# Performance work log

Measured on AMD Instinct MI355X. Metric: run time of the kernel, lower is better.

Reference implementation:

```python
import jax, jax.numpy as jnp
import numpy as np
from jax import lax

B, W, K = 64, 128, 64      # batch, window_size, n_features
KS = 7                      # conv kernel size
EF = W                      # feature-attn embed dim (defaults to window_size, GATv1)
ET = 2 * K                  # temporal-attn embed dim (n_features doubled by GATv2)
H = 256                     # GRU hidden
FH = 256                    # forecast MLP hidden
ALPHA = 0.2                 # leaky relu slope


def _leaky(v):
    return jnp.where(v >= 0, v, ALPHA * v)


def setup_inputs() -> dict:
    key = jax.random.key(0)
    ks = jax.random.split(key, 20)
    s = 0.05
    inp = {
        "x": jax.random.normal(ks[0], (B, W, K), jnp.float32),
        # ConvLayer
        "conv_w": jax.random.normal(ks[1], (K, K, KS), jnp.float32) * s,
        "conv_b": jnp.zeros((K,), jnp.float32),
        # FeatureAttentionLayer (GATv1): lin W->EF, a:[2EF,1], bias [K,K]
        "feat_lin_w": jax.random.normal(ks[2], (EF, W), jnp.float32) * s,
        "feat_lin_b": jnp.zeros((EF,), jnp.float32),
        "feat_a": jax.random.normal(ks[3], (2 * EF, 1), jnp.float32) * s,
        "feat_bias": jnp.zeros((K, K), jnp.float32),
        # TemporalAttentionLayer (GATv2): lin 2K->ET, a:[ET,1], bias [W,W]
        "temp_lin_w": jax.random.normal(ks[4], (ET, 2 * K), jnp.float32) * s,
        "temp_lin_b": jnp.zeros((ET,), jnp.float32),
        "temp_a": jax.random.normal(ks[5], (ET, 1), jnp.float32) * s,
        "temp_bias": jnp.zeros((W, W), jnp.float32),
        # GRU (1 layer), input dim 3K
        "gru_wih": jax.random.normal(ks[6], (3 * H, 3 * K), jnp.float32) * s,
        "gru_whh": jax.random.normal(ks[7], (3 * H, H), jnp.float32) * s,
        "gru_bih": jnp.zeros((3 * H,), jnp.float32),
        "gru_bhh": jnp.zeros((3 * H,), jnp.float32),
        "fc0_w": jax.random.normal(ks[8], (FH, H), jnp.float32) * s,
        "fc0_b": jnp.zeros((FH,), jnp.float32),
        "fc1_w": jax.random.normal(ks[9], (FH, FH), jnp.float32) * s,
        "fc1_b": jnp.zeros((FH,), jnp.float32),
        "fc2_w": jax.random.normal(ks[10], (FH, FH), jnp.float32) * s,
        "fc2_b": jnp.zeros((FH,), jnp.float32),
        "fc3_w": jax.random.normal(ks[11], (K, FH), jnp.float32) * s,
        "fc3_b": jnp.zeros((K,), jnp.float32),
    }
    return inp


def _forward(x, conv_w, conv_b, feat_lin_w, feat_lin_b, feat_a, feat_bias,
             temp_lin_w, temp_lin_b, temp_a, temp_bias,
             gru_wih, gru_whh, gru_bih, gru_bhh,
             fc0_w, fc0_b, fc1_w, fc1_b, fc2_w, fc2_b, fc3_w, fc3_b):
    # --- ConvLayer: pad (k-1)//2 both sides, Conv1d K->K, ReLU ---
    pad = (KS - 1) // 2
    xc = x.transpose(0, 2, 1)                                   # [B,K,W]
    xc = jnp.pad(xc, ((0, 0), (0, 0), (pad, pad)))
    y = lax.conv_general_dilated(xc, conv_w, (1,), 'VALID',
                                 dimension_numbers=('NCH', 'OIH', 'NCH'))
    y = jax.nn.relu(y + conv_b[None, :, None]).transpose(0, 2, 1)  # [B,W,K]

    # --- FeatureAttentionLayer (GATv1): e_ij = leaky((Wx_i||Wx_j)·a) ---
    xf = y.transpose(0, 2, 1)                                   # [B,K,W]
    Wx = xf @ feat_lin_w.T + feat_lin_b                         # [B,K,EF]
    s1 = Wx @ feat_a[:EF, 0]                                    # [B,K]
    s2 = Wx @ feat_a[EF:, 0]                                    # [B,K]
    e_f = _leaky(s1[:, :, None] + s2[:, None, :]) + feat_bias   # [B,K,K]
    att_f = jax.nn.softmax(e_f, axis=2)
    h_feat = jax.nn.sigmoid(att_f @ xf).transpose(0, 2, 1)      # [B,W,K]

    # --- TemporalAttentionLayer (GATv2): g = leaky(lin(x_i||x_j)); e = g·a ---
    W1, W2 = temp_lin_w[:, :K], temp_lin_w[:, K:]               # split lin over concat halves
    p = y @ W1.T                                                # [B,W,ET]
    q = y @ W2.T                                                # [B,W,ET]
    g = _leaky(p[:, :, None, :] + q[:, None, :, :] + temp_lin_b)  # [B,W,W,ET]
    e_t = (g @ temp_a)[..., 0] + temp_bias                      # [B,W,W]
    att_t = jax.nn.softmax(e_t, axis=2)
    h_temp = jax.nn.sigmoid(att_t @ y)                          # [B,W,K]

    # --- concat + GRU over time ---
    z = jnp.concatenate([y, h_feat, h_temp], axis=2)            # [B,W,3K]

    def gru_step(h, xt):
        gi = xt @ gru_wih.T + gru_bih                           # [B,3H]
        gh = h @ gru_whh.T + gru_bhh
        ir, iz, inn = jnp.split(gi, 3, axis=1)
        hr, hz, hn = jnp.split(gh, 3, axis=1)
        r = jax.nn.sigmoid(ir + hr)
        zg = jax.nn.sigmoid(iz + hz)
        n = jnp.tanh(inn + r * hn)
        return (1.0 - zg) * n + zg * h, None

    h0 = jnp.zeros((z.shape[0], H), z.dtype)
    h_end, _ = lax.scan(gru_step, h0, z.transpose(1, 0, 2))     # [B,H]

    # --- Forecasting MLP (eval mode: dropout is identity) ---
    v = jax.nn.relu(h_end @ fc0_w.T + fc0_b)
    v = jax.nn.relu(v @ fc1_w.T + fc1_b)
    v = jax.nn.relu(v @ fc2_w.T + fc2_b)
    return v @ fc3_w.T + fc3_b                                  # [B,K]


def reference(x, conv_w, conv_b, feat_lin_w, feat_lin_b, feat_a, feat_bias,
              temp_lin_w, temp_lin_b, temp_a, temp_bias,
              gru_wih, gru_whh, gru_bih, gru_bhh,
              fc0_w, fc0_b, fc1_w, fc1_b, fc2_w, fc2_b, fc3_w, fc3_b):
    return _forward(x, conv_w, conv_b, feat_lin_w, feat_lin_b, feat_a, feat_bias,
                    temp_lin_w, temp_lin_b, temp_a, temp_bias,
                    gru_wih, gru_whh, gru_bih, gru_bhh,
                    fc0_w, fc0_b, fc1_w, fc1_b, fc2_w, fc2_b, fc3_w, fc3_b)
```

## Files before the change

### kernel.cpp

```cpp
#include <hip/hip_runtime.h>
#include <hip/hip_bf16.h>

typedef unsigned int uint;
typedef _Float16 half2_t __attribute__((ext_vector_type(2)));
typedef _Float16 half8 __attribute__((ext_vector_type(8)));
typedef float f32x4 __attribute__((ext_vector_type(4)));

union H2U { uint u; half2_t h; };
union U4H8 { uint4 u; half8 h; };

#define OFF_Y    0u
#define OFF_Z    524288u
#define OFF_GI   2097152u
#define OFF_WHH  8388608u
#define OFF_C12  8486912u
#define OFF_DD   8487168u
#define OFF_HEND 8487424u

__global__ __launch_bounds__(256) void k_pack_prep(const float* __restrict__ whh, uint* __restrict__ w16,
                                                   const float* __restrict__ flw, const float* __restrict__ flb,
                                                   const float* __restrict__ fa, float* __restrict__ c12,
                                                   float* __restrict__ dd) {
    __shared__ float red[256];
    int bx = blockIdx.x, tid = threadIdx.x;
    if (bx < 384) {
        int idx = bx * 256 + tid;
        int tidq = idx / 384;
        int rem = idx - tidq * 384;
        int u = rem >> 5;
        int q = (rem >> 2) & 7;
        int p = rem & 3;
        int w = tidq >> 6, l = tidq & 63;
        int row = w * 192 + u * 16 + (l & 15);
        int colb = q * 32 + (l >> 4) * 8 + 2 * p;
        float a = whh[(size_t)row * 256 + colb];
        float b = whh[(size_t)row * 256 + colb + 1];
        H2U uu; uu.h.x = (_Float16)a; uu.h.y = (_Float16)b;
        w16[idx] = uu.u;
    } else {
        if (tid < 128) {
            float a = 0.f, b = 0.f;
            for (int e = 0; e < 128; ++e) {
                float w = flw[e * 128 + tid];
                a = fmaf(w, fa[e], a);
                b = fmaf(w, fa[128 + e], b);
            }
            c12[tid] = a;
            c12[128 + tid] = b;
        }
        int e = tid & 127;
        red[tid] = (tid < 128) ? flb[e] * fa[e] : flb[e] * fa[128 + e];
        __syncthreads();
        if (tid < 2) {
            float s = 0.f;
            for (int q = 0; q < 128; ++q) s += red[tid * 128 + q];
            dd[tid] = s;
        }
    }
}

__global__ __launch_bounds__(256) void k_conv(const float* __restrict__ x, const float* __restrict__ cw,
                                              const float* __restrict__ cb, float* __restrict__ y,
                                              float* __restrict__ z) {
    __shared__ float xT[64][41];
    __shared__ float cwL[64 * 64 * 7];
    int b = blockIdx.y, w0 = blockIdx.x * 32, tid = threadIdx.x;
    for (int idx = tid; idx < 38 * 64; idx += 256) {
        int wl = idx / 64, k = idx % 64;
        int wg = w0 - 3 + wl;
        xT[k][wl] = (wg >= 0 && wg < 128) ? x[((size_t)b * 128 + wg) * 64 + k] : 0.f;
    }
    for (int idx = tid; idx < 64 * 64 * 7; idx += 256) cwL[idx] = cw[idx];
    __syncthreads();
    int w_l = tid % 32, kog = tid / 32;
    float acc[8];
#pragma unroll
    for (int i = 0; i < 8; ++i) acc[i] = 0.f;
    for (int ki = 0; ki < 64; ++ki) {
        float x7[7];
#pragma unroll
        for (int u = 0; u < 7; ++u) x7[u] = xT[ki][w_l + u];
#pragma unroll
        for (int koi = 0; koi < 8; ++koi) {
            const float* wp = &cwL[((kog * 8 + koi) * 64 + ki) * 7];
#pragma unroll
            for (int u = 0; u < 7; ++u) acc[koi] = fmaf(x7[u], wp[u], acc[koi]);
        }
    }
    int w = w0 + w_l;
#pragma unroll
    for (int koi = 0; koi < 8; ++koi) {
        int ko = kog * 8 + koi;
        float v = acc[koi] + cb[ko];
        v = v > 0.f ? v : 0.f;
        y[((size_t)b * 128 + w) * 64 + ko] = v;
        z[((size_t)b * 128 + w) * 192 + ko] = v;
    }
}

__global__ __launch_bounds__(256) void k_feat(const float* __restrict__ y, const float* __restrict__ c12,
                                              const float* __restrict__ dd, const float* __restrict__ fb,
                                              float* __restrict__ z) {
    int b = blockIdx.y, w0 = blockIdx.x * 32, tid = threadIdx.x;
    __shared__ float s1L[64], s2L[64];
    __shared__ float attL[64][65];
    __shared__ float yL[32][64];
    __shared__ float cL[256];
    cL[tid] = c12[tid];
    for (int idx = tid; idx < 32 * 64; idx += 256) {
        int wl = idx / 64, j = idx % 64;
        yL[wl][j] = y[((size_t)b * 128 + w0 + wl) * 64 + j];
    }
    __syncthreads();
    if (tid < 128) {
        int k = tid % 64;
        const float* c = (tid < 64) ? cL : cL + 128;
        float acc = 0.f;
        for (int w = 0; w < 128; ++w) acc = fmaf(y[((size_t)b * 128 + w) * 64 + k], c[w], acc);
        if (tid < 64) s1L[k] = acc + dd[0]; else s2L[k] = acc + dd[1];
    }
    __syncthreads();
    if (tid < 64) {
        int k = tid;
        float s1 = s1L[k];
        float m = -1e30f;
        for (int j = 0; j < 64; ++j) {
            float v = s1 + s2L[j];
            float l = fmaxf(v, 0.2f * v);
            float e = l + fb[k * 64 + j];
            attL[k][j] = e;
            m = fmaxf(m, e);
        }
        float s = 0.f;
        for (int j = 0; j < 64; ++j) { float e = __expf(attL[k][j] - m); attL[k][j] = e; s += e; }
        float inv = 1.f / s;
        for (int j = 0; j < 64; ++j) attL[k][j] *= inv;
    }
    __syncthreads();
    int k_l = tid % 64, wg = tid / 64;
    for (int wi = 0; wi < 8; ++wi) {
        int wl = wg * 8 + wi;
        float acc = 0.f;
#pragma unroll 16
        for (int j = 0; j < 64; ++j) acc = fmaf(attL[k_l][j], yL[wl][j], acc);
        float hv = 1.f / (1.f + __expf(-acc));
        z[((size_t)b * 128 + w0 + wl) * 192 + 64 + k_l] = hv;
    }
}

__global__ __launch_bounds__(512) void k_temp(const float* __restrict__ y, const float* __restrict__ tlw,
                                              const float* __restrict__ tlb, const float* __restrict__ ta,
                                              const float* __restrict__ tbias, float* __restrict__ z) {
    int b = blockIdx.y, i0 = blockIdx.x * 32, tid = threadIdx.x;
    __shared__ __align__(16) float yT[64][132];
    __shared__ __align__(16) float qL[128][128];
    __shared__ __align__(16) float pL[32][128];
    __shared__ __align__(16) float etL[32][128];
    __shared__ __align__(16) float taL[128];
    __shared__ float mred[32][8], sred[32][8];
    __shared__ float mrow[32], invL[32];
    if (tid < 128) taL[tid] = ta[tid];
    for (int idx = tid; idx < 8192; idx += 512) {
        int j = idx >> 6, k = idx & 63;
        yT[k][j] = y[((size_t)b * 128 + j) * 64 + k];
    }
    __syncthreads();
    {
        int c = tid & 127, ih = tid >> 7;
        float w1r[64];
        const float4* w1p = (const float4*)(tlw + c * 128);
#pragma unroll
        for (int q4 = 0; q4 < 16; ++q4) {
            float4 v = w1p[q4];
            w1r[4 * q4] = v.x; w1r[4 * q4 + 1] = v.y; w1r[4 * q4 + 2] = v.z; w1r[4 * q4 + 3] = v.w;
        }
        float base = tlb[c];
#pragma unroll
        for (int ilb = 0; ilb < 2; ++ilb) {
            int j0 = i0 + ih * 8 + ilb * 4;
            float4 acc = {base, base, base, base};
            for (int k = 0; k < 64; ++k) {
                float4 yv = *((const float4*)&yT[k][j0]);
                float w = w1r[k];
                acc.x = fmaf(yv.x, w, acc.x); acc.y = fmaf(yv.y, w, acc.y);
                acc.z = fmaf(yv.z, w, acc.z); acc.w = fmaf(yv.w, w, acc.w);
            }
            int il = ih * 8 + ilb * 4;
            pL[il][c] = acc.x; pL[il + 1][c] = acc.y; pL[il + 2][c] = acc.z; pL[il + 3][c] = acc.w;
        }
    }
    {
        int j = tid & 127, ch = tid >> 7;
        float yreg[64];
#pragma unroll
        for (int k = 0; k < 64; ++k) yreg[k] = yT[k][j];
        for (int cc = 0; cc < 32; ++cc) {
            int c = __builtin_amdgcn_readfirstlane(ch * 32 + cc);
            const float* w2 = tlw + c * 128 + 64;
            float acc = 0.f;
#pragma unroll
            for (int k = 0; k < 64; ++k) acc = fmaf(yreg[k], w2[k], acc);
            qL[c][j] = acc;
        }
    }
    __syncthreads();
    {
        int jg = tid & 31, ih = tid >> 5;
        int j0 = jg * 4;
        int il0 = ih * 2;
        float4 acc0 = *((const float4*)(tbias + (size_t)(i0 + il0) * 128 + j0));
        float4 acc1 = *((const float4*)(tbias + (size_t)(i0 + il0 + 1) * 128 + j0));
        for (int c0 = 0; c0 < 128; c0 += 4) {
            float4 ta4 = *((const float4*)&taL[c0]);
            float4 p0 = *((const float4*)&pL[il0][c0]);
            float4 p1 = *((const float4*)&pL[il0 + 1][c0]);
            float4 q0 = *((const float4*)&qL[c0 + 0][j0]);
            float4 q1 = *((const float4*)&qL[c0 + 1][j0]);
            float4 q2 = *((const float4*)&qL[c0 + 2][j0]);
            float4 q3 = *((const float4*)&qL[c0 + 3][j0]);
#define ETSTEP(qv, tac, pa, pb) { \
            float u; \
            u = (pa) + qv.x; acc0.x = fmaf(fmaxf(u, 0.2f * u), (tac), acc0.x); \
            u = (pa) + qv.y; acc0.y = fmaf(fmaxf(u, 0.2f * u), (tac), acc0.y); \
            u = (pa) + qv.z; acc0.z = fmaf(fmaxf(u, 0.2f * u), (tac), acc0.z); \
            u = (pa) + qv.w; acc0.w = fmaf(fmaxf(u, 0.2f * u), (tac), acc0.w); \
            u = (pb) + qv.x; acc1.x = fmaf(fmaxf(u, 0.2f * u), (tac), acc1.x); \
            u = (pb) + qv.y; acc1.y = fmaf(fmaxf(u, 0.2f * u), (tac), acc1.y); \
            u = (pb) + qv.z; acc1.z = fmaf(fmaxf(u, 0.2f * u), (tac), acc1.z); \
            u = (pb) + qv.w; acc1.w = fmaf(fmaxf(u, 0.2f * u), (tac), acc1.w); }
            ETSTEP(q0, ta4.x, p0.x, p1.x)
            ETSTEP(q1, ta4.y, p0.y, p1.y)
            ETSTEP(q2, ta4.z, p0.z, p1.z)
            ETSTEP(q3, ta4.w, p0.w, p1.w)
#undef ETSTEP
        }
        *((float4*)&etL[il0][j0]) = acc0;
        *((float4*)&etL[il0 + 1][j0]) = acc1;
    }
    __syncthreads();
    if (tid < 256) {
        int il = tid >> 3, seg = tid & 7;
        const float4* ep = (const float4*)&etL[il][seg * 16];
        float m = -1e30f;
#pragma unroll
        for (int q = 0; q < 4; ++q) {
            float4 e = ep[q];
            m = fmaxf(m, fmaxf(fmaxf(e.x, e.y), fmaxf(e.z, e.w)));
        }
        mred[il][seg] = m;
    }
    __syncthreads();
    if (tid < 32) {
        float m = mred[tid][0];
#pragma unroll
        for (int s = 1; s < 8; ++s) m = fmaxf(m, mred[tid][s]);
        mrow[tid] = m;
    }
    __syncthreads();
    if (tid < 256) {
        int il = tid >> 3, seg = tid & 7;
        float m = mrow[il];
        float4* ep = (float4*)&etL[il][seg * 16];
        float s = 0.f;
#pragma unroll
        for (int q = 0; q < 4; ++q) {
            float4 e = ep[q];
            e.x = __expf(e.x - m); e.y = __expf(e.y - m);
            e.z = __expf(e.z - m); e.w = __expf(e.w - m);
            s += (e.x + e.y) + (e.z + e.w);
            ep[q] = e;
        }
        sred[il][seg] = s;
    }
    __syncthreads();
    if (tid < 32) {
        float s = 0.f;
#pragma unroll
        for (int q = 0; q < 8; ++q) s += sred[tid][q];
        invL[tid] = 1.f / s;
    }
    __syncthreads();
    {
        int k = tid & 63, ig = tid >> 6;
        float acc[4] = {0.f, 0.f, 0.f, 0.f};
        const float* yb = y + (size_t)b * 128 * 64 + k;
        for (int j0 = 0; j0 < 128; j0 += 4) {
            float yv[4];
#pragma unroll
            for (int jj = 0; jj < 4; ++jj) yv[jj] = yb[(size_t)(j0 + jj) * 64];
#pragma unroll
            for (int ii = 0; ii < 4; ++ii) {
                int il = ig * 4 + ii;
                float4 ev = *((const float4*)&etL[il][j0]);
                acc[ii] = fmaf(ev.x, yv[0], acc[ii]);
                acc[ii] = fmaf(ev.y, yv[1], acc[ii]);
                acc[ii] = fmaf(ev.z, yv[2], acc[ii]);
                acc[ii] = fmaf(ev.w, yv[3], acc[ii]);
            }
        }
#pragma unroll
        for (int ii = 0; ii < 4; ++ii) {
            int il = ig * 4 + ii;
            float hv = 1.f / (1.f + __expf(-acc[ii] * invL[il]));
            z[((size_t)b * 128 + i0 + il) * 192 + 128 + k] = hv;
        }
    }
}

__global__ __launch_bounds__(256) void k_gi(const float* __restrict__ z, const float* __restrict__ wih,
                                            const float* __restrict__ bih, float* __restrict__ gi) {
    int o0 = blockIdx.x * 128;
    int bt0 = blockIdx.y * 64;
    int tid = threadIdx.x;
    __shared__ __align__(16) float zL[64][68];
    __shared__ float wL[128][65];
    int ol = tid & 31;
    int r8 = (tid >> 5) * 8;
    float acc[8][4];
#pragma unroll
    for (int rr = 0; rr < 8; ++rr)
#pragma unroll
        for (int oo = 0; oo < 4; ++oo) acc[rr][oo] = 0.f;
    for (int mc = 0; mc < 3; ++mc) {
        int m0 = mc * 64;
        __syncthreads();
        {
            int mq = (tid & 15) * 4;
            int r = tid >> 4;
#pragma unroll
            for (int it = 0; it < 4; ++it, r += 16) {
                float4 v = *((const float4*)&z[(size_t)(bt0 + r) * 192 + m0 + mq]);
                *((float4*)&zL[r][mq]) = v;
            }
            int o = tid >> 4;
#pragma unroll
            for (int it = 0; it < 8; ++it, o += 16) {
                float4 v = *((const float4*)&wih[(size_t)(o0 + o) * 192 + m0 + mq]);
                wL[o][mq] = v.x; wL[o][mq + 1] = v.y; wL[o][mq + 2] = v.z; wL[o][mq + 3] = v.w;
            }
        }
        __syncthreads();
        for (int mb = 0; mb < 64; mb += 4) {
            float4 zv[8];
#pragma unroll
            for (int rr = 0; rr < 8; ++rr) zv[rr] = *((const float4*)&zL[r8 + rr][mb]);
#pragma unroll
            for (int mi = 0; mi < 4; ++mi) {
                float wv[4];
#pragma unroll
                for (int oo = 0; oo < 4; ++oo) wv[oo] = wL[ol + 32 * oo][mb + mi];
#pragma unroll
                for (int rr = 0; rr < 8; ++rr) {
                    float zc = (mi == 0) ? zv[rr].x : (mi == 1) ? zv[rr].y : (mi == 2) ? zv[rr].z : zv[rr].w;
#pragma unroll
                    for (int oo = 0; oo < 4; ++oo) acc[rr][oo] = fmaf(zc, wv[oo], acc[rr][oo]);
                }
            }
        }
    }
    float bo[4];
#pragma unroll
    for (int oo = 0; oo < 4; ++oo) bo[oo] = bih[o0 + ol + 32 * oo];
#pragma unroll
    for (int rr = 0; rr < 8; ++rr)
#pragma unroll
        for (int oo = 0; oo < 4; ++oo)
            gi[(size_t)(bt0 + r8 + rr) * 768 + o0 + ol + 32 * oo] = acc[rr][oo] + bo[oo];
}

__global__ __launch_bounds__(256)
__attribute__((amdgpu_waves_per_eu(1, 1)))
void k_gru(const float* __restrict__ gi,
           const uint* __restrict__ w16,
           const float* __restrict__ bhh,
           float* __restrict__ hend) {
    int b = blockIdx.x, tid = threadIdx.x;
    int w = tid >> 6, l = tid & 63;
    int quad = l >> 4;
    __shared__ __align__(16) _Float16 hp16[256];
    __shared__ float sH[768];
    half8 bfr[96];
    {
        const uint4* wp4 = (const uint4*)(w16 + (size_t)tid * 384);
#pragma unroll
        for (int i = 0; i < 96; ++i) { U4H8 c_; c_.u = wp4[i]; bfr[i] = c_.h; }
    }
    float br = bhh[tid], bz = bhh[256 + tid], bn = bhh[512 + tid];
    float h = 0.f;
    if (tid < 128) ((uint*)hp16)[tid] = 0u;
    __syncthreads();
    const float* gib = gi + (size_t)b * 128 * 768;
    const uint4* hp4 = (const uint4*)hp16;
    for (int s = 0; s < 128; ++s) {
        float gr = gib[s * 768 + tid];
        float gz = gib[s * 768 + 256 + tid];
        float gn = gib[s * 768 + 512 + tid];
        f32x4 acc[12];
#pragma unroll
        for (int u = 0; u < 12; ++u) acc[u] = (f32x4){0.f, 0.f, 0.f, 0.f};
#pragma unroll
        for (int q = 0; q < 8; ++q) {
            U4H8 c_; c_.u = hp4[q * 4 + quad];
            half8 av = c_.h;
#pragma unroll
            for (int u = 0; u < 12; ++u)
                acc[u] = __builtin_amdgcn_mfma_f32_16x16x32_f16(av, bfr[u * 8 + q], acc[u], 0, 0, 0);
        }
        if (l < 16) {
            int base = w * 192 + l;
#pragma unroll
            for (int u = 0; u < 12; ++u) sH[base + u * 16] = acc[u][0];
        }
        __syncthreads();
        {
            float hr = sH[tid] + br;
            float hz = sH[256 + tid] + bz;
            float hn = sH[512 + tid] + bn;
            float r  = 1.f / (1.f + __expf(-(gr + hr)));
            float zg = 1.f / (1.f + __expf(-(gz + hz)));
            float nx = gn + r * hn;
            float n  = 1.f - 2.f / (1.f + __expf(2.f * nx));
            h = (1.f - zg) * n + zg * h;
            hp16[tid] = (_Float16)h;
        }
        __syncthreads();
    }
    hend[b * 256 + tid] = h;
}

__global__ __launch_bounds__(256) void k_fc(const float* __restrict__ hend,
                                            const float* __restrict__ w0, const float* __restrict__ b0,
                                            const float* __restrict__ w1, const float* __restrict__ b1,
                                            const float* __restrict__ w2, const float* __restrict__ b2,
                                            const float* __restrict__ w3, const float* __restrict__ b3,
                                            float* __restrict__ out) {
    int b = blockIdx.x, tid = threadIdx.x;
    __shared__ float bufA[256], bufB[256];
    bufA[tid] = hend[b * 256 + tid];
    __syncthreads();
    {
        float acc = b0[tid];
        const float* wrow = &w0[tid * 256];
#pragma unroll 8
        for (int m = 0; m < 256; ++m) acc = fmaf(wrow[m], bufA[m], acc);
        bufB[tid] = fmaxf(acc, 0.f);
    }
    __syncthreads();
    {
        float acc = b1[tid];
        const float* wrow = &w1[tid * 256];
#pragma unroll 8
        for (int m = 0; m < 256; ++m) acc = fmaf(wrow[m], bufB[m], acc);
        bufA[tid] = fmaxf(acc, 0.f);
    }
    __syncthreads();
    {
        float acc = b2[tid];
        const float* wrow = &w2[tid * 256];
#pragma unroll 8
        for (int m = 0; m < 256; ++m) acc = fmaf(wrow[m], bufA[m], acc);
        bufB[tid] = fmaxf(acc, 0.f);
    }
    __syncthreads();
    if (tid < 64) {
        float acc = b3[tid];
        const float* wrow = &w3[tid * 256];
#pragma unroll 8
        for (int m = 0; m < 256; ++m) acc = fmaf(wrow[m], bufB[m], acc);
        out[b * 64 + tid] = acc;
    }
}

extern "C" void kernel_launch(void* const* d_in, const int* in_sizes, int n_in,
                              void* d_out, int out_size, void* d_ws, size_t ws_size,
                              hipStream_t stream) {
    const float* x    = (const float*)d_in[0];
    const float* cw   = (const float*)d_in[1];
    const float* cb   = (const float*)d_in[2];
    const float* flw  = (const float*)d_in[3];
    const float* flb  = (const float*)d_in[4];
    const float* fa   = (const float*)d_in[5];
    const float* fb   = (const float*)d_in[6];
    const float* tlw  = (const float*)d_in[7];
    const float* tlb  = (const float*)d_in[8];
    const float* ta   = (const float*)d_in[9];
    const float* tb   = (const float*)d_in[10];
    const float* wih  = (const float*)d_in[11];
    const float* whh  = (const float*)d_in[12];
    const float* bih  = (const float*)d_in[13];
    const float* bhh  = (const float*)d_in[14];
    const float* fc0w = (const float*)d_in[15];
    const float* fc0b = (const float*)d_in[16];
    const float* fc1w = (const float*)d_in[17];
    const float* fc1b = (const float*)d_in[18];
    const float* fc2w = (const float*)d_in[19];
    const float* fc2b = (const float*)d_in[20];
    const float* fc3w = (const float*)d_in[21];
    const float* fc3b = (const float*)d_in[22];

    float* wsf  = (float*)d_ws;
    float* y    = wsf + OFF_Y;
    float* z    = wsf + OFF_Z;
    float* gi   = wsf + OFF_GI;
    uint*  w16  = (uint*)(wsf + OFF_WHH);
    float* c12  = wsf + OFF_C12;
    float* dd   = wsf + OFF_DD;
    float* hend = wsf + OFF_HEND;
    float* out  = (float*)d_out;

    k_pack_prep<<<385, 256, 0, stream>>>(whh, w16, flw, flb, fa, c12, dd);
    k_conv<<<dim3(4, 64), 256, 0, stream>>>(x, cw, cb, y, z);
    k_feat<<<dim3(4, 64), 256, 0, stream>>>(y, c12, dd, fb, z);
    k_temp<<<dim3(4, 64), 512, 0, stream>>>(y, tlw, tlb, ta, tb, z);
    k_gi<<<dim3(6, 128), 256, 0, stream>>>(z, wih, bih, gi);
    k_gru<<<64, 256, 0, stream>>>(gi, w16, bhh, hend);
    k_fc<<<64, 256, 0, stream>>>(hend, fc0w, fc0b, fc1w, fc1b, fc2w, fc2b, fc3w, fc3b, out);
}
```

Before: 475.8 us.

## Pin GRU weights in AGPRs via inline-asm MFMA and restructure temporal Q projection

```diff
diff --git a/kernel.cpp b/kernel.cpp
--- a/kernel.cpp
+++ b/kernel.cpp
@@ -5,9 +5,9 @@
 typedef _Float16 half2_t __attribute__((ext_vector_type(2)));
 typedef _Float16 half8 __attribute__((ext_vector_type(8)));
 typedef float f32x4 __attribute__((ext_vector_type(4)));
+typedef uint u32x4 __attribute__((ext_vector_type(4)));
 
 union H2U { uint u; half2_t h; };
-union U4H8 { uint4 u; half8 h; };
 
 #define OFF_Y    0u
 #define OFF_Z    524288u
@@ -153,7 +153,7 @@
                                               const float* __restrict__ tbias, float* __restrict__ z) {
     int b = blockIdx.y, i0 = blockIdx.x * 32, tid = threadIdx.x;
     __shared__ __align__(16) float yT[64][132];
-    __shared__ __align__(16) float qL[128][128];
+    __shared__ __align__(16) float qL[128][132];
     __shared__ __align__(16) float pL[32][128];
     __shared__ __align__(16) float etL[32][128];
     __shared__ __align__(16) float taL[128];
@@ -190,17 +190,25 @@
         }
     }
     {
-        int j = tid & 127, ch = tid >> 7;
-        float yreg[64];
-#pragma unroll
-        for (int k = 0; k < 64; ++k) yreg[k] = yT[k][j];
-        for (int cc = 0; cc < 32; ++cc) {
-            int c = __builtin_amdgcn_readfirstlane(ch * 32 + cc);
-            const float* w2 = tlw + c * 128 + 64;
-            float acc = 0.f;
-#pragma unroll
-            for (int k = 0; k < 64; ++k) acc = fmaf(yreg[k], w2[k], acc);
-            qL[c][j] = acc;
+        int c = tid & 127, ih = tid >> 7;
+        float w2r[64];
+        const float4* w2p = (const float4*)(tlw + c * 128 + 64);
+#pragma unroll
+        for (int q4 = 0; q4 < 16; ++q4) {
+            float4 v = w2p[q4];
+            w2r[4 * q4] = v.x; w2r[4 * q4 + 1] = v.y; w2r[4 * q4 + 2] = v.z; w2r[4 * q4 + 3] = v.w;
+        }
+#pragma unroll
+        for (int jq = 0; jq < 8; ++jq) {
+            int j0 = ih * 32 + jq * 4;
+            float4 acc = {0.f, 0.f, 0.f, 0.f};
+            for (int k = 0; k < 64; ++k) {
+                float4 yv = *((const float4*)&yT[k][j0]);
+                float w = w2r[k];
+                acc.x = fmaf(yv.x, w, acc.x); acc.y = fmaf(yv.y, w, acc.y);
+                acc.z = fmaf(yv.z, w, acc.z); acc.w = fmaf(yv.w, w, acc.w);
+            }
+            *((float4*)&qL[c][j0]) = acc;
         }
     }
     __syncthreads();
@@ -379,18 +387,19 @@
     int quad = l >> 4;
     __shared__ __align__(16) _Float16 hp16[256];
     __shared__ float sH[768];
-    half8 bfr[96];
-    {
-        const uint4* wp4 = (const uint4*)(w16 + (size_t)tid * 384);
-#pragma unroll
-        for (int i = 0; i < 96; ++i) { U4H8 c_; c_.u = wp4[i]; bfr[i] = c_.h; }
+    u32x4 wq[96];
+    {
+        const u32x4* wp4 = (const u32x4*)(w16 + (size_t)tid * 384);
+#pragma unroll
+        for (int i = 0; i < 96; ++i) wq[i] = wp4[i];
     }
     float br = bhh[tid], bz = bhh[256 + tid], bn = bhh[512 + tid];
     float h = 0.f;
     if (tid < 128) ((uint*)hp16)[tid] = 0u;
     __syncthreads();
     const float* gib = gi + (size_t)b * 128 * 768;
-    const uint4* hp4 = (const uint4*)hp16;
+    const _Float16* hq = hp16 + quad * 8;
+    int sbase = w * 192 + l;
     for (int s = 0; s < 128; ++s) {
         float gr = gib[s * 768 + tid];
         float gz = gib[s * 768 + 256 + tid];
@@ -400,16 +409,33 @@
         for (int u = 0; u < 12; ++u) acc[u] = (f32x4){0.f, 0.f, 0.f, 0.f};
 #pragma unroll
         for (int q = 0; q < 8; ++q) {
-            U4H8 c_; c_.u = hp4[q * 4 + quad];
-            half8 av = c_.h;
-#pragma unroll
-            for (int u = 0; u < 12; ++u)
-                acc[u] = __builtin_amdgcn_mfma_f32_16x16x32_f16(av, bfr[u * 8 + q], acc[u], 0, 0, 0);
+            u32x4 avu = *((const u32x4*)(hq + q * 32));
+            asm volatile(
+                "v_mfma_f32_16x16x32_f16 %0, %12, %13, %0\n\t"
+                "v_mfma_f32_16x16x32_f16 %1, %12, %14, %1\n\t"
+                "v_mfma_f32_16x16x32_f16 %2, %12, %15, %2\n\t"
+                "v_mfma_f32_16x16x32_f16 %3, %12, %16, %3\n\t"
+                "v_mfma_f32_16x16x32_f16 %4, %12, %17, %4\n\t"
+                "v_mfma_f32_16x16x32_f16 %5, %12, %18, %5\n\t"
+                "v_mfma_f32_16x16x32_f16 %6, %12, %19, %6\n\t"
+                "v_mfma_f32_16x16x32_f16 %7, %12, %20, %7\n\t"
+                "v_mfma_f32_16x16x32_f16 %8, %12, %21, %8\n\t"
+                "v_mfma_f32_16x16x32_f16 %9, %12, %22, %9\n\t"
+                "v_mfma_f32_16x16x32_f16 %10, %12, %23, %10\n\t"
+                "v_mfma_f32_16x16x32_f16 %11, %12, %24, %11\n\t"
+                "s_nop 7\n\t"
+                "s_nop 7\n\t"
+                : "+v"(acc[0]), "+v"(acc[1]), "+v"(acc[2]), "+v"(acc[3]),
+                  "+v"(acc[4]), "+v"(acc[5]), "+v"(acc[6]), "+v"(acc[7]),
+                  "+v"(acc[8]), "+v"(acc[9]), "+v"(acc[10]), "+v"(acc[11])
+                : "v"(avu),
+                  "a"(wq[0 * 8 + q]), "a"(wq[1 * 8 + q]), "a"(wq[2 * 8 + q]), "a"(wq[3 * 8 + q]),
+                  "a"(wq[4 * 8 + q]), "a"(wq[5 * 8 + q]), "a"(wq[6 * 8 + q]), "a"(wq[7 * 8 + q]),
+                  "v"(wq[8 * 8 + q]), "v"(wq[9 * 8 + q]), "v"(wq[10 * 8 + q]), "v"(wq[11 * 8 + q]));
         }
         if (l < 16) {
-            int base = w * 192 + l;
-#pragma unroll
-            for (int u = 0; u < 12; ++u) sH[base + u * 16] = acc[u][0];
+#pragma unroll
+            for (int u = 0; u < 12; ++u) sH[sbase + u * 16] = acc[u][0];
         }
         __syncthreads();
         {
```

New measurement: 443.5 us. 6.8% less time.
